# Kernel tuning notes

Hardware: AMD Instinct MI355X
Metric: run time of the kernel (lower is better)

Reference implementation:

```python
import jax, jax.numpy as jnp
import numpy as np

K, N, F_IN, F_HID, F_OUT = 4, 8192, 128, 64, 16
DROPOUT_P = 0.3


def setup_inputs() -> dict:
    key = jax.random.key(0)
    ks = jax.random.split(key, 8)
    return {
        "adj": jax.random.uniform(ks[0], (K, N, N), dtype=jnp.float32),
        "x": jax.random.normal(ks[1], (N, F_IN), dtype=jnp.float32),
        "W1": jax.random.normal(ks[2], (F_IN, F_HID), dtype=jnp.float32) * 0.05,
        "b1": jax.random.normal(ks[3], (F_HID,), dtype=jnp.float32) * 0.05,
        "W2": jax.random.normal(ks[4], (F_HID, F_OUT), dtype=jnp.float32) * 0.05,
        "b2": jax.random.normal(ks[5], (F_OUT,), dtype=jnp.float32) * 0.05,
        "pi1": jax.random.normal(ks[6], (K,), dtype=jnp.float32),
        "pi2": jax.random.normal(ks[7], (K,), dtype=jnp.float32),
    }


def _gconv(adj, x, W, b, pi):
    # mixed adjacency: [N, N] = sum_k pi[k] * adj[k]
    A = jnp.einsum('k,knm->nm', pi, adj)
    support = x @ W                     # [N, F_out]
    return A @ support + b              # [N, F_out]


def reference(adj, x, W1, b1, W2, b2, pi1, pi2):
    # gc1.pi is softmax-normalized in Co_GCN.forward
    pi1_n = jax.nn.softmax(pi1)
    h = jax.nn.relu(_gconv(adj, x, W1, b1, pi1_n))   # [N, F_HID]
    # F.dropout with p=0.3, training=True (functional default): fixed-key mask
    keep = jax.random.bernoulli(jax.random.key(42), 1.0 - DROPOUT_P, h.shape)
    h = jnp.where(keep, h / (1.0 - DROPOUT_P), 0.0)
    out = _gconv(adj, h, W2, b2, pi2)                # [N, F_OUT]
    return out
```

## Files before the change

kernel.cpp:

```cpp
#include <hip/hip_runtime.h>
#include <stdint.h>

#define NN 8192
#define FIN 128
#define FH 64
#define FO 16
#define BM 64
#define BN 64
#define SPLIT 8
#define NRANGE (NN / SPLIT)
#define NCHUNK (NRANGE / BN)

typedef float    f32x4 __attribute__((ext_vector_type(4)));
typedef _Float16 f16x4 __attribute__((ext_vector_type(4)));

static __device__ __forceinline__ void fma4(float4& acc, float a, const float4 s) {
  acc.x = fmaf(a, s.x, acc.x);
  acc.y = fmaf(a, s.y, acc.y);
  acc.z = fmaf(a, s.z, acc.z);
  acc.w = fmaf(a, s.w, acc.w);
}

__global__ __launch_bounds__(256) void k_s1(const float* __restrict__ x,
                                            const float* __restrict__ W1,
                                            float* __restrict__ S1) {
  __shared__ float W1l[FIN * FH];
  __shared__ float xl[16][FIN + 4];
  const int t = threadIdx.x;
  const int n0 = blockIdx.x * 16;
  for (int i = t; i < FIN * FH / 4; i += 256)
    ((float4*)W1l)[i] = ((const float4*)W1)[i];
  for (int i = t; i < 16 * FIN; i += 256) {
    int r = i >> 7, c = i & (FIN - 1);
    xl[r][c] = x[(size_t)(n0 + r) * FIN + c];
  }
  __syncthreads();
  const int m = t >> 4;
  const int j0 = (t & 15) << 2;
  float4 acc = {0.f, 0.f, 0.f, 0.f};
#pragma unroll 8
  for (int k = 0; k < FIN; ++k) {
    float xv = xl[m][k];
    float4 w = *(const float4*)&W1l[k * FH + j0];
    fma4(acc, xv, w);
  }
  *(float4*)&S1[(size_t)(n0 + m) * FH + j0] = acc;
}

__global__ __launch_bounds__(256, 4) void k_pass1_fused(const float* __restrict__ adj,
                                                        const float* __restrict__ S1,
                                                        const float* __restrict__ pi1,
                                                        const float* __restrict__ pi2,
                                                        float* __restrict__ hpart,
                                                        _Float16* __restrict__ A2h) {
  __shared__ float Alds[BN][BM];
  __shared__ float S1l[BN][FH];
  const int t = threadIdx.x;
  const int mb = blockIdx.x >> 3;
  const int sp = blockIdx.x & 7;

  float p0 = pi1[0], p1 = pi1[1], p2 = pi1[2], p3 = pi1[3];
  float mx = fmaxf(fmaxf(p0, p1), fmaxf(p2, p3));
  float e0 = expf(p0 - mx), e1 = expf(p1 - mx), e2 = expf(p2 - mx), e3 = expf(p3 - mx);
  float inv = 1.0f / (e0 + e1 + e2 + e3);
  const float w0 = e0 * inv, w1 = e1 * inv, w2 = e2 * inv, w3 = e3 * inv;
  const float v0 = pi2[0], v1 = pi2[1], v2 = pi2[2], v3 = pi2[3];

  const size_t NN2 = (size_t)NN * NN;
  const size_t row0 = (size_t)mb * BM;
  const int nbase = sp * NRANGE;

  const int n4 = t & 15;
  const int ms = t >> 4;
  const int m0 = (t & 15) << 2;
  const int j0 = (t >> 4) << 2;

  f32x4 pf[4][4];
  f32x4 pfS[4];

  float4 acc0 = {0,0,0,0}, acc1 = {0,0,0,0}, acc2 = {0,0,0,0}, acc3 = {0,0,0,0};

  auto ISSUE = [&](int c) {
    const int n0 = nbase + c * BN;
#pragma unroll
    for (int p = 0; p < 4; ++p) {
      const float* g = adj + (row0 + (size_t)(ms + (p << 4))) * NN + (size_t)(n0 + (n4 << 2));
      pf[p][0] = __builtin_nontemporal_load((const f32x4*)g);
      pf[p][1] = __builtin_nontemporal_load((const f32x4*)(g + NN2));
      pf[p][2] = __builtin_nontemporal_load((const f32x4*)(g + 2 * NN2));
      pf[p][3] = __builtin_nontemporal_load((const f32x4*)(g + 3 * NN2));
    }
    const f32x4* src = (const f32x4*)(S1 + (size_t)n0 * FH);
#pragma unroll
    for (int i = 0; i < 4; ++i) pfS[i] = src[t + 256 * i];
  };

  auto STAGE = [&](int c) {
    const int n0 = nbase + c * BN;
#pragma unroll
    for (int p = 0; p < 4; ++p) {
      const int ml = ms + (p << 4);
      const int mc = ml ^ (n4 << 2);
      f32x4 a0 = pf[p][0], a1 = pf[p][1], a2 = pf[p][2], a3 = pf[p][3];
      Alds[(n4 << 2) + 0][mc] = fmaf(w0, a0.x, fmaf(w1, a1.x, fmaf(w2, a2.x, w3 * a3.x)));
      Alds[(n4 << 2) + 1][mc] = fmaf(w0, a0.y, fmaf(w1, a1.y, fmaf(w2, a2.y, w3 * a3.y)));
      Alds[(n4 << 2) + 2][mc] = fmaf(w0, a0.z, fmaf(w1, a1.z, fmaf(w2, a2.z, w3 * a3.z)));
      Alds[(n4 << 2) + 3][mc] = fmaf(w0, a0.w, fmaf(w1, a1.w, fmaf(w2, a2.w, w3 * a3.w)));
      f16x4 h4;
      h4.x = (_Float16)fmaf(v0, a0.x, fmaf(v1, a1.x, fmaf(v2, a2.x, v3 * a3.x)));
      h4.y = (_Float16)fmaf(v0, a0.y, fmaf(v1, a1.y, fmaf(v2, a2.y, v3 * a3.y)));
      h4.z = (_Float16)fmaf(v0, a0.z, fmaf(v1, a1.z, fmaf(v2, a2.z, v3 * a3.z)));
      h4.w = (_Float16)fmaf(v0, a0.w, fmaf(v1, a1.w, fmaf(v2, a2.w, v3 * a3.w)));
      __builtin_nontemporal_store(h4, (f16x4*)(A2h + (row0 + (size_t)ml) * NN + (size_t)(n0 + (n4 << 2))));
    }
    f32x4* dst = (f32x4*)&S1l[0][0];
#pragma unroll
    for (int i = 0; i < 4; ++i) dst[t + 256 * i] = pfS[i];
  };

  ISSUE(0);
  for (int c = 0; c < NCHUNK; ++c) {
    __syncthreads();
    STAGE(c);
    if (c + 1 < NCHUNK) ISSUE(c + 1);
    asm volatile("s_waitcnt lgkmcnt(0)" ::: "memory");
    __builtin_amdgcn_s_barrier();
#pragma unroll 4
    for (int n = 0; n < BN; ++n) {
      const float4 a = *(const float4*)&Alds[n][m0 ^ (n & 60)];
      const float4 s = *(const float4*)&S1l[n][j0];
      fma4(acc0, a.x, s);
      fma4(acc1, a.y, s);
      fma4(acc2, a.z, s);
      fma4(acc3, a.w, s);
    }
  }
  float* hp = hpart + (size_t)sp * NN * FH;
  const size_t rbase = (row0 + m0) * FH + j0;
  *(float4*)&hp[rbase]          = acc0;
  *(float4*)&hp[rbase + FH]     = acc1;
  *(float4*)&hp[rbase + 2 * FH] = acc2;
  *(float4*)&hp[rbase + 3 * FH] = acc3;
}

__device__ __forceinline__ float dropout_scale(uint32_t e) {
  uint32_t x0 = 0u;
  uint32_t x1 = e;
  const uint32_t ks1 = 42u;
  const uint32_t ks2 = 0x1BD11BF0u;
  x1 += ks1;
#define TFR(d) { x0 += x1; x1 = (x1 << d) | (x1 >> (32 - d)); x1 ^= x0; }
  TFR(13) TFR(15) TFR(26) TFR(6)   x0 += ks1; x1 += ks2 + 1u;
  TFR(17) TFR(29) TFR(16) TFR(24)  x0 += ks2; x1 += 0u  + 2u;
  TFR(13) TFR(15) TFR(26) TFR(6)   x0 += 0u;  x1 += ks1 + 3u;
  TFR(17) TFR(29) TFR(16) TFR(24)  x0 += ks1; x1 += ks2 + 4u;
  TFR(13) TFR(15) TFR(26) TFR(6)   x0 += ks2; x1 += 0u  + 5u;
#undef TFR
  uint32_t bits = x0 ^ x1;
  float u = __uint_as_float((bits >> 9) | 0x3f800000u) - 1.0f;
  return (u < 0.7f) ? (1.0f / 0.7f) : 0.0f;
}

__global__ __launch_bounds__(256) void k_mid(const float* __restrict__ hpart,
                                             const float* __restrict__ b1,
                                             const float* __restrict__ W2,
                                             float* __restrict__ HW) {
  __shared__ float hl[4][FH];
  __shared__ float W2l[FH * FO];
  const int t = threadIdx.x;
  const int n0 = blockIdx.x << 2;
  for (int i = t; i < FH * FO; i += 256) W2l[i] = W2[i];
  const int j = t & 63, r = t >> 6;
  const uint32_t idx = (uint32_t)(n0 + r) * FH + j;
  const size_t NF = (size_t)NN * FH;
  float pre = b1[j];
#pragma unroll
  for (int s = 0; s < SPLIT; ++s) pre += hpart[idx + (size_t)s * NF];
  float v = fmaxf(pre, 0.0f) * dropout_scale(idx);
  hl[r][j] = v;
  __syncthreads();
  if (t < 64) {
    const int rr = t >> 4, f = t & 15;
    float s = 0.f;
#pragma unroll 8
    for (int jj = 0; jj < FH; ++jj)
      s = fmaf(hl[rr][jj], W2l[jj * FO + f], s);
    HW[(size_t)(n0 + rr) * FO + f] = s;
  }
}

__global__ __launch_bounds__(256, 4) void k_pass2_half(const _Float16* __restrict__ A2h,
                                                       const float* __restrict__ HW,
                                                       float* __restrict__ opart) {
  __shared__ float Alds[BN][BM];
  __shared__ float HWl[BN * FO];
  const int t = threadIdx.x;
  const int mb = blockIdx.x >> 3;
  const int sp = blockIdx.x & 7;

  const size_t row0 = (size_t)mb * BM;
  const int nbase = sp * NRANGE;

  const int n4 = t & 15;
  const int ms = t >> 4;
  const int m0 = (t & 15) << 2;
  const int f  = t >> 4;

  f16x4 pf[4];
  f32x4 pfH;

  float4 acc = {0,0,0,0};

  auto ISSUE = [&](int c) {
    const int n0 = nbase + c * BN;
#pragma unroll
    for (int p = 0; p < 4; ++p)
      pf[p] = *(const f16x4*)(A2h + (row0 + (size_t)(ms + (p << 4))) * NN + (size_t)(n0 + (n4 << 2)));
    pfH = ((const f32x4*)(HW + (size_t)n0 * FO))[t];
  };

  auto STAGE = [&]() {
#pragma unroll
    for (int p = 0; p < 4; ++p) {
      const int mc = (ms + (p << 4)) ^ (n4 << 2);
      Alds[(n4 << 2) + 0][mc] = (float)pf[p].x;
      Alds[(n4 << 2) + 1][mc] = (float)pf[p].y;
      Alds[(n4 << 2) + 2][mc] = (float)pf[p].z;
      Alds[(n4 << 2) + 3][mc] = (float)pf[p].w;
    }
    ((f32x4*)HWl)[t] = pfH;
  };

  ISSUE(0);
  for (int c = 0; c < NCHUNK; ++c) {
    __syncthreads();
    STAGE();
    if (c + 1 < NCHUNK) ISSUE(c + 1);
    asm volatile("s_waitcnt lgkmcnt(0)" ::: "memory");
    __builtin_amdgcn_s_barrier();
#pragma unroll 4
    for (int n = 0; n < BN; ++n) {
      const float4 a = *(const float4*)&Alds[n][m0 ^ (n & 60)];
      const float hv = HWl[n * FO + f];
      acc.x = fmaf(a.x, hv, acc.x);
      acc.y = fmaf(a.y, hv, acc.y);
      acc.z = fmaf(a.z, hv, acc.z);
      acc.w = fmaf(a.w, hv, acc.w);
    }
  }
  float* op = opart + (size_t)sp * NN * FO;
  const size_t r = (row0 + m0) * FO + f;
  op[r]          = acc.x;
  op[r + FO]     = acc.y;
  op[r + 2 * FO] = acc.z;
  op[r + 3 * FO] = acc.w;
}

__global__ __launch_bounds__(256) void k_fin(const float* __restrict__ opart,
                                             const float* __restrict__ b2,
                                             float* __restrict__ out) {
  const int e = blockIdx.x * 256 + threadIdx.x;
  const size_t NFo = (size_t)NN * FO;
  float s = b2[e & 15];
#pragma unroll
  for (int p = 0; p < SPLIT; ++p) s += opart[e + (size_t)p * NFo];
  out[e] = s;
}

extern "C" void kernel_launch(void* const* d_in, const int* in_sizes, int n_in,
                              void* d_out, int out_size, void* d_ws, size_t ws_size,
                              hipStream_t stream) {
  const float* adj = (const float*)d_in[0];
  const float* x   = (const float*)d_in[1];
  const float* W1  = (const float*)d_in[2];
  const float* b1  = (const float*)d_in[3];
  const float* W2  = (const float*)d_in[4];
  const float* b2  = (const float*)d_in[5];
  const float* pi1 = (const float*)d_in[6];
  const float* pi2 = (const float*)d_in[7];
  float* out = (float*)d_out;
  float* ws  = (float*)d_ws;

  float* S1    = ws;
  float* hpart = S1 + (size_t)NN * FH;
  float* HW    = hpart + (size_t)SPLIT * NN * FH;
  float* opart = HW + (size_t)NN * FO;
  _Float16* A2h = (_Float16*)(opart + (size_t)SPLIT * NN * FO);

  k_s1         <<<NN / 16,           256, 0, stream>>>(x, W1, S1);
  k_pass1_fused<<<(NN / BM) * SPLIT, 256, 0, stream>>>(adj, S1, pi1, pi2, hpart, A2h);
  k_mid        <<<NN / 4,            256, 0, stream>>>(hpart, b1, W2, HW);
  k_pass2_half <<<(NN / BM) * SPLIT, 256, 0, stream>>>(A2h, HW, opart);
  k_fin        <<<(NN * FO) / 256,   256, 0, stream>>>(opart, b2, out);
}
```

Measured before the change: 355.2 us.

## Rewrite second aggregation as fp16 dot2 kernel with atomic accumulation

```diff
diff --git a/kernel.cpp b/kernel.cpp
--- a/kernel.cpp
+++ b/kernel.cpp
@@ -7,18 +7,36 @@
 #define FO 16
 #define BM 64
 #define BN 64
-#define SPLIT 8
-#define NRANGE (NN / SPLIT)
-#define NCHUNK (NRANGE / BN)
+#define SPLIT1 4
+#define NRANGE1 (NN / SPLIT1)
+#define NCHUNK1 (NRANGE1 / BN)
+#define SPLIT2 16
+#define NRANGE2 (NN / SPLIT2)
 
 typedef float    f32x4 __attribute__((ext_vector_type(4)));
 typedef _Float16 f16x4 __attribute__((ext_vector_type(4)));
+typedef _Float16 f16x8 __attribute__((ext_vector_type(8)));
+typedef _Float16 h2    __attribute__((ext_vector_type(2)));
+
+union U8 { f16x8 v; h2 p[4]; };
 
 static __device__ __forceinline__ void fma4(float4& acc, float a, const float4 s) {
   acc.x = fmaf(a, s.x, acc.x);
   acc.y = fmaf(a, s.y, acc.y);
   acc.z = fmaf(a, s.z, acc.z);
   acc.w = fmaf(a, s.w, acc.w);
+}
+
+static __device__ __forceinline__ float dot2(h2 a, h2 b, float c) {
+#if defined(__has_builtin)
+#if __has_builtin(__builtin_amdgcn_fdot2)
+  return __builtin_amdgcn_fdot2(a, b, c, false);
+#else
+  return c + (float)a.x * (float)b.x + (float)a.y * (float)b.y;
+#endif
+#else
+  return c + (float)a.x * (float)b.x + (float)a.y * (float)b.y;
+#endif
 }
 
 __global__ __launch_bounds__(256) void k_s1(const float* __restrict__ x,
@@ -47,17 +65,17 @@
   *(float4*)&S1[(size_t)(n0 + m) * FH + j0] = acc;
 }
 
-__global__ __launch_bounds__(256, 4) void k_pass1_fused(const float* __restrict__ adj,
-                                                        const float* __restrict__ S1,
-                                                        const float* __restrict__ pi1,
-                                                        const float* __restrict__ pi2,
-                                                        float* __restrict__ hpart,
-                                                        _Float16* __restrict__ A2h) {
+__global__ __launch_bounds__(256) void k_pass1_fused(const float* __restrict__ adj,
+                                                     const float* __restrict__ S1,
+                                                     const float* __restrict__ pi1,
+                                                     const float* __restrict__ pi2,
+                                                     float* __restrict__ hpart,
+                                                     _Float16* __restrict__ A2h) {
   __shared__ float Alds[BN][BM];
   __shared__ float S1l[BN][FH];
   const int t = threadIdx.x;
-  const int mb = blockIdx.x >> 3;
-  const int sp = blockIdx.x & 7;
+  const int mb = blockIdx.x >> 2;
+  const int sp = blockIdx.x & 3;
 
   float p0 = pi1[0], p1 = pi1[1], p2 = pi1[2], p3 = pi1[3];
   float mx = fmaxf(fmaxf(p0, p1), fmaxf(p2, p3));
@@ -68,7 +86,7 @@
 
   const size_t NN2 = (size_t)NN * NN;
   const size_t row0 = (size_t)mb * BM;
-  const int nbase = sp * NRANGE;
+  const int nbase = sp * NRANGE1;
 
   const int n4 = t & 15;
   const int ms = t >> 4;
@@ -111,7 +129,7 @@
       h4.y = (_Float16)fmaf(v0, a0.y, fmaf(v1, a1.y, fmaf(v2, a2.y, v3 * a3.y)));
       h4.z = (_Float16)fmaf(v0, a0.z, fmaf(v1, a1.z, fmaf(v2, a2.z, v3 * a3.z)));
       h4.w = (_Float16)fmaf(v0, a0.w, fmaf(v1, a1.w, fmaf(v2, a2.w, v3 * a3.w)));
-      __builtin_nontemporal_store(h4, (f16x4*)(A2h + (row0 + (size_t)ml) * NN + (size_t)(n0 + (n4 << 2))));
+      *(f16x4*)(A2h + (row0 + (size_t)ml) * NN + (size_t)(n0 + (n4 << 2))) = h4;
     }
     f32x4* dst = (f32x4*)&S1l[0][0];
 #pragma unroll
@@ -119,10 +137,10 @@
   };
 
   ISSUE(0);
-  for (int c = 0; c < NCHUNK; ++c) {
+  for (int c = 0; c < NCHUNK1; ++c) {
     __syncthreads();
     STAGE(c);
-    if (c + 1 < NCHUNK) ISSUE(c + 1);
+    if (c + 1 < NCHUNK1) ISSUE(c + 1);
     asm volatile("s_waitcnt lgkmcnt(0)" ::: "memory");
     __builtin_amdgcn_s_barrier();
 #pragma unroll 4
@@ -164,7 +182,7 @@
 __global__ __launch_bounds__(256) void k_mid(const float* __restrict__ hpart,
                                              const float* __restrict__ b1,
                                              const float* __restrict__ W2,
-                                             float* __restrict__ HW) {
+                                             _Float16* __restrict__ HWT) {
   __shared__ float hl[4][FH];
   __shared__ float W2l[FH * FO];
   const int t = threadIdx.x;
@@ -175,7 +193,7 @@
   const size_t NF = (size_t)NN * FH;
   float pre = b1[j];
 #pragma unroll
-  for (int s = 0; s < SPLIT; ++s) pre += hpart[idx + (size_t)s * NF];
+  for (int s = 0; s < SPLIT1; ++s) pre += hpart[idx + (size_t)s * NF];
   float v = fmaxf(pre, 0.0f) * dropout_scale(idx);
   hl[r][j] = v;
   __syncthreads();
@@ -185,86 +203,90 @@
 #pragma unroll 8
     for (int jj = 0; jj < FH; ++jj)
       s = fmaf(hl[rr][jj], W2l[jj * FO + f], s);
-    HW[(size_t)(n0 + rr) * FO + f] = s;
-  }
-}
-
-__global__ __launch_bounds__(256, 4) void k_pass2_half(const _Float16* __restrict__ A2h,
-                                                       const float* __restrict__ HW,
-                                                       float* __restrict__ opart) {
-  __shared__ float Alds[BN][BM];
-  __shared__ float HWl[BN * FO];
+    HWT[(size_t)f * NN + (n0 + rr)] = (_Float16)s;
+  }
+}
+
+__global__ __launch_bounds__(256) void k_init(const float* __restrict__ b2,
+                                              float* __restrict__ out) {
+  const int e = blockIdx.x * 256 + threadIdx.x;
+  out[e] = b2[e & 15];
+}
+
+__global__ __launch_bounds__(64) void k_pass2_dot(const _Float16* __restrict__ A2h,
+                                                  const _Float16* __restrict__ HWT,
+                                                  float* __restrict__ out) {
+  __shared__ f16x8 Htl[64 * 16];
   const int t = threadIdx.x;
-  const int mb = blockIdx.x >> 3;
-  const int sp = blockIdx.x & 7;
-
+  const int mb = blockIdx.x >> 4;
+  const int sp = blockIdx.x & 15;
   const size_t row0 = (size_t)mb * BM;
-  const int nbase = sp * NRANGE;
-
-  const int n4 = t & 15;
-  const int ms = t >> 4;
-  const int m0 = (t & 15) << 2;
-  const int f  = t >> 4;
-
-  f16x4 pf[4];
-  f32x4 pfH;
-
-  float4 acc = {0,0,0,0};
-
-  auto ISSUE = [&](int c) {
-    const int n0 = nbase + c * BN;
-#pragma unroll
-    for (int p = 0; p < 4; ++p)
-      pf[p] = *(const f16x4*)(A2h + (row0 + (size_t)(ms + (p << 4))) * NN + (size_t)(n0 + (n4 << 2)));
-    pfH = ((const f32x4*)(HW + (size_t)n0 * FO))[t];
-  };
-
-  auto STAGE = [&]() {
-#pragma unroll
-    for (int p = 0; p < 4; ++p) {
-      const int mc = (ms + (p << 4)) ^ (n4 << 2);
-      Alds[(n4 << 2) + 0][mc] = (float)pf[p].x;
-      Alds[(n4 << 2) + 1][mc] = (float)pf[p].y;
-      Alds[(n4 << 2) + 2][mc] = (float)pf[p].z;
-      Alds[(n4 << 2) + 3][mc] = (float)pf[p].w;
+  const int nbase = sp * NRANGE2;
+
+#pragma unroll
+  for (int i = 0; i < FO; ++i)
+    Htl[t * FO + i] = *(const f16x8*)(HWT + (size_t)i * NN + nbase + t * 8);
+  __syncthreads();
+
+  const int fgrp = t & 3;
+  const int mgrp = t >> 2;
+  const size_t rbase = (row0 + (size_t)mgrp * 4) * NN + nbase;
+
+  float acc[4][4];
+#pragma unroll
+  for (int j = 0; j < 4; ++j)
+#pragma unroll
+    for (int i = 0; i < 4; ++i) acc[j][i] = 0.f;
+
+  f16x8 aA[4], aB[4];
+#pragma unroll
+  for (int j = 0; j < 4; ++j)
+    aA[j] = *(const f16x8*)(A2h + rbase + (size_t)j * NN);
+
+  auto LOADB = [&](int o) {
+#pragma unroll
+    for (int j = 0; j < 4; ++j)
+      aB[j] = *(const f16x8*)(A2h + rbase + (size_t)j * NN + o * 8);
+  };
+  auto LOADA = [&](int o) {
+#pragma unroll
+    for (int j = 0; j < 4; ++j)
+      aA[j] = *(const f16x8*)(A2h + rbase + (size_t)j * NN + o * 8);
+  };
+
+  auto COMPUTE = [&](const f16x8* buf, int o) {
+    U8 h0, h1, h2v, h3;
+    h0.v  = Htl[o * FO + fgrp * 4 + 0];
+    h1.v  = Htl[o * FO + fgrp * 4 + 1];
+    h2v.v = Htl[o * FO + fgrp * 4 + 2];
+    h3.v  = Htl[o * FO + fgrp * 4 + 3];
+#pragma unroll
+    for (int j = 0; j < 4; ++j) {
+      U8 a;
+      a.v = buf[j];
+#pragma unroll
+      for (int q = 0; q < 4; ++q) {
+        h2 pa = a.p[q];
+        acc[j][0] = dot2(pa, h0.p[q],  acc[j][0]);
+        acc[j][1] = dot2(pa, h1.p[q],  acc[j][1]);
+        acc[j][2] = dot2(pa, h2v.p[q], acc[j][2]);
+        acc[j][3] = dot2(pa, h3.p[q],  acc[j][3]);
+      }
     }
-    ((f32x4*)HWl)[t] = pfH;
-  };
-
-  ISSUE(0);
-  for (int c = 0; c < NCHUNK; ++c) {
-    __syncthreads();
-    STAGE();
-    if (c + 1 < NCHUNK) ISSUE(c + 1);
-    asm volatile("s_waitcnt lgkmcnt(0)" ::: "memory");
-    __builtin_amdgcn_s_barrier();
-#pragma unroll 4
-    for (int n = 0; n < BN; ++n) {
-      const float4 a = *(const float4*)&Alds[n][m0 ^ (n & 60)];
-      const float hv = HWl[n * FO + f];
-      acc.x = fmaf(a.x, hv, acc.x);
-      acc.y = fmaf(a.y, hv, acc.y);
-      acc.z = fmaf(a.z, hv, acc.z);
-      acc.w = fmaf(a.w, hv, acc.w);
-    }
-  }
-  float* op = opart + (size_t)sp * NN * FO;
-  const size_t r = (row0 + m0) * FO + f;
-  op[r]          = acc.x;
-  op[r + FO]     = acc.y;
-  op[r + 2 * FO] = acc.z;
-  op[r + 3 * FO] = acc.w;
-}
-
-__global__ __launch_bounds__(256) void k_fin(const float* __restrict__ opart,
-                                             const float* __restrict__ b2,
-                                             float* __restrict__ out) {
-  const int e = blockIdx.x * 256 + threadIdx.x;
-  const size_t NFo = (size_t)NN * FO;
-  float s = b2[e & 15];
-#pragma unroll
-  for (int p = 0; p < SPLIT; ++p) s += opart[e + (size_t)p * NFo];
-  out[e] = s;
+  };
+
+  for (int o = 0; o < 64; o += 2) {
+    LOADB(o + 1);
+    COMPUTE(aA, o);
+    if (o + 2 < 64) LOADA(o + 2);
+    COMPUTE(aB, o + 1);
+  }
+
+#pragma unroll
+  for (int j = 0; j < 4; ++j)
+#pragma unroll
+    for (int i = 0; i < 4; ++i)
+      atomicAdd(&out[(row0 + (size_t)mgrp * 4 + j) * FO + fgrp * 4 + i], acc[j][i]);
 }
 
 extern "C" void kernel_launch(void* const* d_in, const int* in_sizes, int n_in,
@@ -283,13 +305,12 @@
 
   float* S1    = ws;
   float* hpart = S1 + (size_t)NN * FH;
-  float* HW    = hpart + (size_t)SPLIT * NN * FH;
-  float* opart = HW + (size_t)NN * FO;
-  _Float16* A2h = (_Float16*)(opart + (size_t)SPLIT * NN * FO);
-
-  k_s1         <<<NN / 16,           256, 0, stream>>>(x, W1, S1);
-  k_pass1_fused<<<(NN / BM) * SPLIT, 256, 0, stream>>>(adj, S1, pi1, pi2, hpart, A2h);
-  k_mid        <<<NN / 4,            256, 0, stream>>>(hpart, b1, W2, HW);
-  k_pass2_half <<<(NN / BM) * SPLIT, 256, 0, stream>>>(A2h, HW, opart);
-  k_fin        <<<(NN * FO) / 256,   256, 0, stream>>>(opart, b2, out);
-}
+  _Float16* A2h = (_Float16*)(hpart + (size_t)SPLIT1 * NN * FH);
+  _Float16* HWT = A2h + (size_t)NN * NN;
+
+  k_s1         <<<NN / 16,            256, 0, stream>>>(x, W1, S1);
+  k_pass1_fused<<<(NN / BM) * SPLIT1, 256, 0, stream>>>(adj, S1, pi1, pi2, hpart, A2h);
+  k_mid        <<<NN / 4,             256, 0, stream>>>(hpart, b1, W2, HWT);
+  k_init       <<<(NN * FO) / 256,    256, 0, stream>>>(b2, out);
+  k_pass2_dot  <<<(NN / BM) * SPLIT2,  64, 0, stream>>>(A2h, HWT, out);
+}
```

Result: no change. 349.2 us (-1.7%).
